# Performance work log

Measured on AMD Instinct MI355X. Metric: run time of the kernel, lower is better.

## Reference

```python
import jax, jax.numpy as jnp
import numpy as np

N_HEADS = 64
N_KV_HEADS = 8
HEAD_DIM = 128
HIDDEN = 8192
SEQ = 2048


def setup_inputs() -> dict:
    key = jax.random.key(0)
    k1, k2, k3, k4 = jax.random.split(key, 4)
    scale = 1.0 / np.sqrt(HIDDEN)
    x = jax.random.normal(k1, (1, 1, SEQ, HIDDEN), dtype=jnp.float32)
    wq = jax.random.normal(k2, (HIDDEN, N_HEADS * HEAD_DIM), dtype=jnp.float32) * scale
    wk = jax.random.normal(k3, (HIDDEN, N_KV_HEADS * HEAD_DIM), dtype=jnp.float32) * scale
    wv = jax.random.normal(k4, (HIDDEN, N_KV_HEADS * HEAD_DIM), dtype=jnp.float32) * scale
    return {"x": x, "wq": wq, "wk": wk, "wv": wv}


def reference(x, wq, wk, wv):
    # Fused QKV projection: concat weights along output dim, single matmul.
    qkv_w = jnp.concatenate([wq, wk, wv], axis=-1)  # [H, (64+8+8)*128]
    fused = jnp.einsum('bush,hd->busd', x, qkv_w)    # [1,1,S,10240]
    b, _, s, _ = fused.shape
    q_dim = N_HEADS * HEAD_DIM
    kv_dim = N_KV_HEADS * HEAD_DIM
    q = fused[..., :q_dim]
    k = fused[..., q_dim:q_dim + kv_dim]
    v = fused[..., q_dim + kv_dim:]
    # nlp_create_qkv_heads: [B,1,S,nh*hd] -> [B,nh,S,hd]
    q_heads = q.reshape(b, s, N_HEADS, HEAD_DIM).transpose(0, 2, 1, 3)
    k_heads = k.reshape(b, s, N_KV_HEADS, HEAD_DIM).transpose(0, 2, 1, 3)
    v_heads = v.reshape(b, s, N_KV_HEADS, HEAD_DIM).transpose(0, 2, 1, 3)
    return (q_heads, k_heads, v_heads)
```

## Files before the change

kernel.cpp:

```cpp
#include <hip/hip_runtime.h>
#include <stdint.h>

#define M_DIM 2048
#define K_DIM 8192
#define N_Q   8192
#define N_KV  1024
#define BM    128
#define BN    128
#define BK    32
#define NIT   (K_DIM / BK)

typedef __bf16 bf16x8 __attribute__((ext_vector_type(8)));
typedef __bf16 bf16x2 __attribute__((ext_vector_type(2)));
typedef float  f32x4  __attribute__((ext_vector_type(4)));

__device__ __forceinline__ uint32_t swz(uint32_t r) { return ((r >> 1) ^ (r >> 3)) & 3u; }

__device__ __forceinline__ uint32_t pack_bf16(float lo, float hi) {
    bf16x2 v = { (__bf16)lo, (__bf16)hi };
    return __builtin_bit_cast(uint32_t, v);
}

__global__ __launch_bounds__(256) void qkv_gemm(
    const float* __restrict__ x,
    const float* __restrict__ wq,
    const float* __restrict__ wk,
    const float* __restrict__ wv,
    float* __restrict__ out)
{
    __shared__ __align__(16) uint16_t sA[BM * BK];
    __shared__ __align__(16) uint16_t sB[BN * BK];
    uint32_t* sAu = (uint32_t*)sA;
    uint32_t* sBu = (uint32_t*)sB;

    const uint32_t tid    = threadIdx.x;
    const uint32_t bid    = blockIdx.x;
    const uint32_t mt_blk = bid & 15;
    const uint32_t nt_blk = bid >> 4;
    const uint32_t m0     = mt_blk * BM;

    const size_t QSZ = (size_t)64 * M_DIM * 128;
    const size_t KSZ = (size_t)8  * M_DIM * 128;
    const float* Wsel;
    uint32_t ldW, col0;
    size_t obase;
    if (nt_blk < 64)      { Wsel = wq; ldW = N_Q;  col0 = nt_blk * 128;
                            obase = (size_t)nt_blk * M_DIM * 128; }
    else if (nt_blk < 72) { Wsel = wk; ldW = N_KV; col0 = (nt_blk - 64) * 128;
                            obase = QSZ + (size_t)(nt_blk - 64) * M_DIM * 128; }
    else                  { Wsel = wv; ldW = N_KV; col0 = (nt_blk - 72) * 128;
                            obase = QSZ + KSZ + (size_t)(nt_blk - 72) * M_DIM * 128; }

    const float* agp = x + (size_t)(m0 + (tid >> 3)) * K_DIM + (tid & 7) * 4;
    uint32_t a_wr[4];
    #pragma unroll
    for (int i = 0; i < 4; ++i) {
        uint32_t r = i * 32 + (tid >> 3);
        a_wr[i] = r * 16 + ((((tid >> 1) & 3) ^ swz(r)) * 4) + (tid & 1) * 2;
    }

    const uint32_t bk  = (tid >> 4) * 2;
    const uint32_t bn0 = (tid & 15) * 8;
    const float* bgp = Wsel + (size_t)bk * ldW + col0 + bn0;
    const uint32_t bkc = bk >> 3;
    const uint32_t bkd = (bk & 7) >> 1;

    f32x4 apre[4], bpre[4];
    #pragma unroll
    for (int i = 0; i < 4; ++i) apre[i] = *(const f32x4*)(agp + (size_t)i * 32 * K_DIM);
    bpre[0] = *(const f32x4*)(bgp);
    bpre[1] = *(const f32x4*)(bgp + 4);
    bpre[2] = *(const f32x4*)(bgp + ldW);
    bpre[3] = *(const f32x4*)(bgp + ldW + 4);

    const uint32_t lane = tid & 63;
    const uint32_t wid  = tid >> 6;
    const uint32_t wm   = (wid >> 1) * 64;
    const uint32_t wn   = (wid & 1) * 64;
    const uint32_t l15  = lane & 15;
    const uint32_t quad = lane >> 4;

    f32x4 acc[4][4] = {};

    uint32_t a_off[4], b_off[4];
    #pragma unroll
    for (int t = 0; t < 4; ++t) {
        uint32_t ar = wm + t * 16 + l15;
        a_off[t] = ar * BK + ((quad ^ swz(ar)) * 8);
        uint32_t br = wn + t * 16 + l15;
        b_off[t] = br * BK + ((quad ^ swz(br)) * 8);
    }

    const float* agp_n = agp + BK;
    const float* bgp_n = bgp + (size_t)BK * ldW;

    for (uint32_t kt = 0; kt < NIT; ++kt) {
        __syncthreads();

        #pragma unroll
        for (int i = 0; i < 4; ++i) {
            uint2 w;
            w.x = pack_bf16(apre[i].x, apre[i].y);
            w.y = pack_bf16(apre[i].z, apre[i].w);
            *(uint2*)&sAu[a_wr[i]] = w;
        }
        {
            const float* pk0 = (const float*)&bpre[0];
            const float* pk1 = (const float*)&bpre[2];
            #pragma unroll
            for (int j = 0; j < 8; ++j) {
                uint32_t n = bn0 + j;
                sBu[n * 16 + ((bkc ^ swz(n)) * 4) + bkd] = pack_bf16(pk0[j], pk1[j]);
            }
        }

        if (kt + 1 < NIT) {
            #pragma unroll
            for (int i = 0; i < 4; ++i) apre[i] = *(const f32x4*)(agp_n + (size_t)i * 32 * K_DIM);
            bpre[0] = *(const f32x4*)(bgp_n);
            bpre[1] = *(const f32x4*)(bgp_n + 4);
            bpre[2] = *(const f32x4*)(bgp_n + ldW);
            bpre[3] = *(const f32x4*)(bgp_n + ldW + 4);
            agp_n += BK;
            bgp_n += (size_t)BK * ldW;
        }

        __syncthreads();

        bf16x8 af[4], bf[4];
        #pragma unroll
        for (int t = 0; t < 4; ++t) {
            af[t] = *(const bf16x8*)(sA + a_off[t]);
            bf[t] = *(const bf16x8*)(sB + b_off[t]);
        }
        #pragma unroll
        for (int mt = 0; mt < 4; ++mt)
            #pragma unroll
            for (int nt = 0; nt < 4; ++nt)
                acc[mt][nt] = __builtin_amdgcn_mfma_f32_16x16x32_bf16(
                    af[mt], bf[nt], acc[mt][nt], 0, 0, 0);
    }

    float* op = out + obase + (size_t)m0 * 128;
    #pragma unroll
    for (int mt = 0; mt < 4; ++mt) {
        #pragma unroll
        for (int r = 0; r < 4; ++r) {
            uint32_t row = wm + mt * 16 + quad * 4 + r;
            #pragma unroll
            for (int nt = 0; nt < 4; ++nt) {
                uint32_t col = wn + nt * 16 + l15;
                op[(size_t)row * 128 + col] = acc[mt][nt][r];
            }
        }
    }
}

extern "C" void kernel_launch(void* const* d_in, const int* in_sizes, int n_in,
                              void* d_out, int out_size, void* d_ws, size_t ws_size,
                              hipStream_t stream) {
    const float* x  = (const float*)d_in[0];
    const float* wq = (const float*)d_in[1];
    const float* wk = (const float*)d_in[2];
    const float* wv = (const float*)d_in[3];
    qkv_gemm<<<dim3((M_DIM / BM) * ((N_Q + 2 * N_KV) / BN)), dim3(256), 0, stream>>>(
        x, wq, wk, wv, (float*)d_out);
}
```

Baseline: 1.019 ms.

## Preconvert x and weights to bf16 and use async LDS loads in GEMM

Adds prepass kernels that convert x to bf16 and transpose-convert the weights into a K-contiguous bf16 buffer in workspace. The GEMM then streams tiles directly into LDS with global_load_lds, removing per-iteration fp32 loads, packing and scattered LDS writes. This adds extra full passes over the inputs and the weights each call. The old kernel is kept as a fallback when the workspace is too small.

```diff
diff --git a/kernel.cpp b/kernel.cpp
--- a/kernel.cpp
+++ b/kernel.cpp
@@ -5,6 +5,7 @@
 #define K_DIM 8192
 #define N_Q   8192
 #define N_KV  1024
+#define N_TOT (N_Q + 2 * N_KV)
 #define BM    128
 #define BN    128
 #define BK    32
@@ -21,7 +22,145 @@
     return __builtin_bit_cast(uint32_t, v);
 }
 
-__global__ __launch_bounds__(256) void qkv_gemm(
+__device__ __forceinline__ void async_copy16(const void* g, void* l) {
+    __builtin_amdgcn_global_load_lds(
+        (const __attribute__((address_space(1))) uint32_t*)g,
+        (__attribute__((address_space(3))) uint32_t*)l, 16, 0, 0);
+}
+
+
+__global__ __launch_bounds__(256) void cvt_x(const float* __restrict__ x,
+                                             uint16_t* __restrict__ xb) {
+    const size_t n4 = (size_t)M_DIM * K_DIM / 4;
+    size_t i = (size_t)blockIdx.x * 256 + threadIdx.x;
+    const size_t stride = (size_t)gridDim.x * 256;
+    for (; i < n4; i += stride) {
+        f32x4 v = ((const f32x4*)x)[i];
+        uint2 w;
+        w.x = pack_bf16(v.x, v.y);
+        w.y = pack_bf16(v.z, v.w);
+        ((uint2*)xb)[i] = w;
+    }
+}
+
+__global__ __launch_bounds__(256) void transpose_w(const float* __restrict__ W,
+                                                   uint16_t* __restrict__ WT,
+                                                   int ldW) {
+    __shared__ float sT[64][65];
+    const uint32_t t  = threadIdx.x;
+    const uint32_t n0 = blockIdx.x * 64;
+    const uint32_t k0 = blockIdx.y * 64;
+
+    const uint32_t kl = t >> 4, nn = (t & 15) * 4;
+    #pragma unroll
+    for (int i = 0; i < 4; ++i) {
+        f32x4 v = *(const f32x4*)(W + (size_t)(k0 + kl + 16 * i) * ldW + n0 + nn);
+        sT[kl + 16 * i][nn + 0] = v.x;
+        sT[kl + 16 * i][nn + 1] = v.y;
+        sT[kl + 16 * i][nn + 2] = v.z;
+        sT[kl + 16 * i][nn + 3] = v.w;
+    }
+    __syncthreads();
+
+    const uint32_t n = t >> 2, kc = (t & 3) * 16;
+    uint32_t d[8];
+    #pragma unroll
+    for (int j = 0; j < 8; ++j)
+        d[j] = pack_bf16(sT[kc + 2 * j][n], sT[kc + 2 * j + 1][n]);
+    uint16_t* op = WT + (size_t)(n0 + n) * K_DIM + k0 + kc;
+    *(uint4*)(op)     = *(uint4*)&d[0];
+    *(uint4*)(op + 8) = *(uint4*)&d[4];
+}
+
+
+__global__ __launch_bounds__(256) void qkv_gemm_bf16(
+    const uint16_t* __restrict__ xb,
+    const uint16_t* __restrict__ wt,
+    float* __restrict__ out)
+{
+    __shared__ __align__(16) uint16_t sA[BM * BK];
+    __shared__ __align__(16) uint16_t sB[BN * BK];
+
+    const uint32_t tid    = threadIdx.x;
+    const uint32_t bid    = blockIdx.x;
+    const uint32_t mt_blk = bid & 15;
+    const uint32_t nt_blk = bid >> 4;
+    const uint32_t m0     = mt_blk * BM;
+    const uint32_t n0     = nt_blk * BN;
+
+    const uint32_t c0 = tid, c1 = tid + 256;
+    const uint32_t r0 = c0 >> 2, r1 = c1 >> 2;
+    const uint32_t kc0 = (c0 & 3) ^ swz(r0);
+    const uint32_t kc1 = (c1 & 3) ^ swz(r1);
+    const uint16_t* agp0 = xb + (size_t)(m0 + r0) * K_DIM + kc0 * 8;
+    const uint16_t* agp1 = xb + (size_t)(m0 + r1) * K_DIM + kc1 * 8;
+    const uint16_t* bgp0 = wt + (size_t)(n0 + r0) * K_DIM + kc0 * 8;
+    const uint16_t* bgp1 = wt + (size_t)(n0 + r1) * K_DIM + kc1 * 8;
+    uint16_t* alds0 = sA + c0 * 8;
+    uint16_t* alds1 = sA + c1 * 8;
+    uint16_t* blds0 = sB + c0 * 8;
+    uint16_t* blds1 = sB + c1 * 8;
+
+    const uint32_t lane = tid & 63;
+    const uint32_t wid  = tid >> 6;
+    const uint32_t wm   = (wid >> 1) * 64;
+    const uint32_t wn   = (wid & 1) * 64;
+    const uint32_t l15  = lane & 15;
+    const uint32_t quad = lane >> 4;
+
+    f32x4 acc[4][4] = {};
+
+    uint32_t a_off[4], b_off[4];
+    #pragma unroll
+    for (int t = 0; t < 4; ++t) {
+        uint32_t ar = wm + t * 16 + l15;
+        a_off[t] = ar * BK + ((quad ^ swz(ar)) * 8);
+        uint32_t br = wn + t * 16 + l15;
+        b_off[t] = br * BK + ((quad ^ swz(br)) * 8);
+    }
+
+    for (uint32_t kt = 0; kt < NIT; ++kt) {
+        __syncthreads();
+
+        const size_t ko = (size_t)kt * BK;
+        async_copy16(agp0 + ko, alds0);
+        async_copy16(agp1 + ko, alds1);
+        async_copy16(bgp0 + ko, blds0);
+        async_copy16(bgp1 + ko, blds1);
+
+        __syncthreads();
+
+        bf16x8 af[4], bf[4];
+        #pragma unroll
+        for (int t = 0; t < 4; ++t) {
+            af[t] = *(const bf16x8*)(sA + a_off[t]);
+            bf[t] = *(const bf16x8*)(sB + b_off[t]);
+        }
+        #pragma unroll
+        for (int mt = 0; mt < 4; ++mt)
+            #pragma unroll
+            for (int nt = 0; nt < 4; ++nt)
+                acc[mt][nt] = __builtin_amdgcn_mfma_f32_16x16x32_bf16(
+                    af[mt], bf[nt], acc[mt][nt], 0, 0, 0);
+    }
+
+    float* op = out + (size_t)nt_blk * M_DIM * 128 + (size_t)m0 * 128;
+    #pragma unroll
+    for (int mt = 0; mt < 4; ++mt) {
+        #pragma unroll
+        for (int r = 0; r < 4; ++r) {
+            uint32_t row = wm + mt * 16 + quad * 4 + r;
+            #pragma unroll
+            for (int nt = 0; nt < 4; ++nt) {
+                uint32_t col = wn + nt * 16 + l15;
+                op[(size_t)row * 128 + col] = acc[mt][nt][r];
+            }
+        }
+    }
+}
+
+
+__global__ __launch_bounds__(256) void qkv_gemm_fb(
     const float* __restrict__ x,
     const float* __restrict__ wq,
     const float* __restrict__ wk,
@@ -156,6 +295,7 @@
     }
 }
 
+
 extern "C" void kernel_launch(void* const* d_in, const int* in_sizes, int n_in,
                               void* d_out, int out_size, void* d_ws, size_t ws_size,
                               hipStream_t stream) {
@@ -163,6 +303,22 @@
     const float* wq = (const float*)d_in[1];
     const float* wk = (const float*)d_in[2];
     const float* wv = (const float*)d_in[3];
-    qkv_gemm<<<dim3((M_DIM / BM) * ((N_Q + 2 * N_KV) / BN)), dim3(256), 0, stream>>>(
-        x, wq, wk, wv, (float*)d_out);
-}
+    float* out = (float*)d_out;
+
+    const size_t xb_bytes = (size_t)M_DIM * K_DIM * 2;
+    const size_t wt_bytes = (size_t)N_TOT * K_DIM * 2;
+    if (ws_size >= xb_bytes + wt_bytes) {
+        uint16_t* xb = (uint16_t*)d_ws;
+        uint16_t* wt = (uint16_t*)((char*)d_ws + xb_bytes);
+        cvt_x<<<dim3(2048), dim3(256), 0, stream>>>(x, xb);
+        transpose_w<<<dim3(N_Q / 64, K_DIM / 64), dim3(256), 0, stream>>>(wq, wt, N_Q);
+        transpose_w<<<dim3(N_KV / 64, K_DIM / 64), dim3(256), 0, stream>>>(
+            wk, wt + (size_t)N_Q * K_DIM, N_KV);
+        transpose_w<<<dim3(N_KV / 64, K_DIM / 64), dim3(256), 0, stream>>>(
+            wv, wt + (size_t)(N_Q + N_KV) * K_DIM, N_KV);
+        qkv_gemm_bf16<<<dim3((M_DIM / BM) * (N_TOT / BN)), dim3(256), 0, stream>>>(xb, wt, out);
+    } else {
+        qkv_gemm_fb<<<dim3((M_DIM / BM) * (N_TOT / BN)), dim3(256), 0, stream>>>(
+            x, wq, wk, wv, out);
+    }
+}
```

Result: slower. 1.063 ms (+4.3%).
